# Kernel optimization log

Measured on AMD Instinct MI355X. Metric: run time of the kernel, lower is better.

The kernel has to match this reference:

```python
import jax, jax.numpy as jnp
import numpy as np

H = 16      # hidden_size (fixed by fc1 = Linear(16, 32))
L = 4       # num_layers
F = 256     # feature_size
A = 16      # attention_hidden_size
T = 131072  # seq_len


def setup_inputs() -> dict:
    key = jax.random.key(0)
    ks = jax.random.split(key, 17)
    def g(k, shape, scale=0.1):
        return jax.random.normal(k, shape, dtype=jnp.float32) * scale
    return {
        "batch": jax.random.normal(ks[0], (T, 1, F), dtype=jnp.float32),
        # GRUCell layer 0 (input F -> H), PyTorch layout [3H, in]: r|z|n gates
        "Wih0": g(ks[1], (3 * H, F)), "Whh0": g(ks[2], (3 * H, H)),
        "bih0": g(ks[3], (3 * H,)),   "bhh0": g(ks[4], (3 * H,)),
        # GRUCell layers 1..L-1 (H -> H), stacked
        "Wih": g(ks[5], (L - 1, 3 * H, H)), "Whh": g(ks[6], (L - 1, 3 * H, H)),
        "bih": g(ks[7], (L - 1, 3 * H)),    "bhh": g(ks[8], (L - 1, 3 * H)),
        # additive self-attention combine per layer: v^T tanh(W h + b) + c
        "aW": g(ks[9], (L, H, A)), "ab": g(ks[10], (L, A)),
        "av": g(ks[11], (L, A)),   "avb": g(ks[12], (L,)),
        # head MLP (dropout = identity in eval)
        "fc1W": g(ks[13], (32, H)), "fc1b": g(ks[14], (32,)),
        "fc2W": g(ks[15], (1, 32)), "fc2b": g(ks[16], (1,)),
    }


def _gru(x, h, Wih, Whh, bih, bhh):
    # PyTorch GRUCell math, gates ordered r|z|n
    gi = x @ Wih.T + bih          # [1, 3H]
    gh = h @ Whh.T + bhh          # [1, 3H]
    ir, iz, inn = jnp.split(gi, 3, axis=-1)
    hr, hz, hn = jnp.split(gh, 3, axis=-1)
    r = jax.nn.sigmoid(ir + hr)
    z = jax.nn.sigmoid(iz + hz)
    n = jnp.tanh(inn + r * hn)
    return (1.0 - z) * n + z * h


def reference(batch, Wih0, Whh0, bih0, bhh0, Wih, Whh, bih, bhh,
              aW, ab, av, avb, fc1W, fc1b, fc2W, fc2b):
    def step(hs, x_t):  # hs: [L, 1, H], x_t: [1, F]
        inp = x_t
        new = []
        for l in range(L):  # fixed tiny layer loop, distinct weights
            if l == 0:
                hn = _gru(inp, hs[0], Wih0, Whh0, bih0, bhh0)
            else:
                hn = _gru(inp, hs[l], Wih[l - 1], Whh[l - 1], bih[l - 1], bhh[l - 1])
            new.append(hn)
            inp = hn
        stack = jnp.stack(new)  # [L, 1, H]
        outs = []
        for i in range(L):
            sub = stack[i:]                                        # [L-i, 1, H]
            s = jnp.tanh(sub @ aW[i] + ab[i]) @ av[i] + avb[i]      # [L-i, 1]
            a = jax.nn.softmax(s, axis=0)
            outs.append(jnp.sum(a[..., None] * sub, axis=0))        # [1, H]
        hs_new = jnp.stack(outs)                                    # [L, 1, H]
        top = hs_new[-1][0]                                         # [H]
        o = jax.nn.relu(top @ fc1W.T + fc1b) @ fc2W.T + fc2b        # [1]
        return hs_new, o

    hs0 = jnp.zeros((L, 1, H), dtype=batch.dtype)
    _, ys = jax.lax.scan(step, hs0, batch)
    return ys  # [T, 1]
```

## Files before the change

### kernel.cpp

```cpp
#include <hip/hip_runtime.h>
#include <cstddef>

namespace {
constexpr int kH = 16;
constexpr int kL = 4;
constexpr int kF = 256;
constexpr int kA = 16;
constexpr int kG = 48;
}

#define PIN(x) asm volatile("" : "+v"(x))

#if defined(__has_builtin)
#if __has_builtin(__builtin_amdgcn_permlane16_swap) && __has_builtin(__builtin_amdgcn_permlane32_swap)
#define HAVE_PLSWAP 1
#endif
#endif

#ifdef HAVE_PLSWAP
__device__ __forceinline__ float swap_sum32(float x) {
  auto r = __builtin_amdgcn_permlane32_swap(__float_as_uint(x), __float_as_uint(x), false, false);
  return __uint_as_float(r[0]) + __uint_as_float(r[1]);
}
__device__ __forceinline__ float swap_sum16(float x) {
  auto r = __builtin_amdgcn_permlane16_swap(__float_as_uint(x), __float_as_uint(x), false, false);
  return __uint_as_float(r[0]) + __uint_as_float(r[1]);
}
#else
__device__ __forceinline__ float swap_sum32(float x) {
  return x + __shfl(x, (int)(threadIdx.x & 63) ^ 32, 64);
}
__device__ __forceinline__ float swap_sum16(float x) {
  return x + __shfl(x, (int)(threadIdx.x & 63) ^ 16, 64);
}
#endif

template <int CTRL>
__device__ __forceinline__ float ror_add(float x) {
  int r = __builtin_amdgcn_update_dpp(0, __float_as_int(x), CTRL, 0xF, 0xF, false);
  return x + __int_as_float(r);
}
__device__ __forceinline__ float row_sum16(float x) {
  x = ror_add<0x128>(x);
  x = ror_add<0x124>(x);
  x = ror_add<0x122>(x);
  x = ror_add<0x121>(x);
  return x;
}
__device__ __forceinline__ float fast_rcp(float x) { return __builtin_amdgcn_rcpf(x); }
constexpr float kL2E = 1.4426950408889634f;
__device__ __forceinline__ float sigm(float x) {
  return fast_rcp(1.0f + __builtin_amdgcn_exp2f(-kL2E * x));
}
__device__ __forceinline__ float tanh_f(float x) {
  return 1.0f - 2.0f * fast_rcp(1.0f + __builtin_amdgcn_exp2f((2.0f * kL2E) * x));
}

#define FMAC_ROR(acc, h, w, J)                                            \
  asm volatile("v_fmac_f32_dpp %0, %1, %2 row_ror:" #J                    \
               " row_mask:0xf bank_mask:0xf"                              \
               : "+v"(acc) : "v"(h), "v"(w))
#define MUL_ROR(dst, h, w, J)                                             \
  asm volatile("v_mul_f32_dpp %0, %1, %2 row_ror:" #J                     \
               " row_mask:0xf bank_mask:0xf"                              \
               : "=v"(dst) : "v"(h), "v"(w))

__device__ __forceinline__ float dot16r(const float* w, float h, float bias) {
  float a0, a1, a2, a3;
  asm volatile("v_fma_f32 %0, %1, %2, %3" : "=v"(a0) : "v"(h), "v"(w[0]), "v"(bias));
  asm volatile("s_nop 0" ::: );
  MUL_ROR(a1, h, w[1], 1);
  MUL_ROR(a2, h, w[2], 2);
  MUL_ROR(a3, h, w[3], 3);
  FMAC_ROR(a0, h, w[4], 4);
  FMAC_ROR(a1, h, w[5], 5);
  FMAC_ROR(a2, h, w[6], 6);
  FMAC_ROR(a3, h, w[7], 7);
  FMAC_ROR(a0, h, w[8], 8);
  FMAC_ROR(a1, h, w[9], 9);
  FMAC_ROR(a2, h, w[10], 10);
  FMAC_ROR(a3, h, w[11], 11);
  FMAC_ROR(a0, h, w[12], 12);
  FMAC_ROR(a1, h, w[13], 13);
  FMAC_ROR(a2, h, w[14], 14);
  FMAC_ROR(a3, h, w[15], 15);
  return (a0 + a1) + (a2 + a3);
}

__global__ __launch_bounds__(256) void gi0_kernel(
    const float* __restrict__ batch, const float* __restrict__ Wih0,
    const float* __restrict__ bih0, float* __restrict__ gi0, int T) {
  __shared__ __align__(16) float w[kG * kF];
  __shared__ float bsh[kG];
  for (int i = threadIdx.x; i < kG * kF; i += blockDim.x) w[i] = Wih0[i];
  if (threadIdx.x < kG) bsh[threadIdx.x] = bih0[threadIdx.x];
  __syncthreads();
  int t = blockIdx.x * blockDim.x + threadIdx.x;
  if (t >= T) return;
  float acc[kG];
#pragma unroll
  for (int gg = 0; gg < kG; ++gg) acc[gg] = bsh[gg];
  const float* brow = batch + (size_t)t * kF;
  for (int f = 0; f < kF; f += 4) {
    const float4 b4 = *reinterpret_cast<const float4*>(brow + f);
#pragma unroll
    for (int gg = 0; gg < kG; ++gg) {
      const float4 w4 = *reinterpret_cast<const float4*>(&w[gg * kF + f]);
      acc[gg] = fmaf(b4.x, w4.x, acc[gg]);
      acc[gg] = fmaf(b4.y, w4.y, acc[gg]);
      acc[gg] = fmaf(b4.z, w4.z, acc[gg]);
      acc[gg] = fmaf(b4.w, w4.w, acc[gg]);
    }
  }
  float* orow = gi0 + (size_t)t * kG;
#pragma unroll
  for (int gg = 0; gg < kG; gg += 4) {
    *reinterpret_cast<float4*>(orow + gg) =
        make_float4(acc[gg], acc[gg + 1], acc[gg + 2], acc[gg + 3]);
  }
}

__global__ __launch_bounds__(64)
__attribute__((amdgpu_waves_per_eu(1, 1)))
void seq_kernel(
    const float* __restrict__ Whh0, const float* __restrict__ bhh0,
    const float* __restrict__ Wih, const float* __restrict__ Whh,
    const float* __restrict__ bih, const float* __restrict__ bhh,
    const float* __restrict__ aW, const float* __restrict__ ab,
    const float* __restrict__ av, const float* __restrict__ avb,
    const float* __restrict__ gi0, float* __restrict__ topout, int T) {
  const int lane = threadIdx.x & 63;
  const int grp = lane >> 4;
  const int a = lane & 15;
  const int gr = (grp == 0) ? a : (grp == 2 ? 32 + a : 16 + a);

  float Wh[kL][kH];
  float Ux[3][kH];
  float aWj[kH];
#pragma unroll
  for (int j = 0; j < kH; ++j) {
    const int idx = (a - j) & 15;
    Wh[0][j] = Whh0[gr * kH + idx];
#pragma unroll
    for (int l = 1; l < kL; ++l) {
      Wh[l][j] = Whh[((l - 1) * kG + gr) * kH + idx];
      Ux[l - 1][j] = Wih[((l - 1) * kG + gr) * kH + idx];
    }
    aWj[j] = aW[(grp * kH + idx) * kA + a];
  }
  float bh[kL], bi[3];
  bh[0] = bhh0[gr];
#pragma unroll
  for (int l = 1; l < kL; ++l) {
    bh[l] = bhh[(l - 1) * kG + gr];
    bi[l - 1] = bih[(l - 1) * kG + gr];
  }
  float abr = ab[grp * kA + a];
  float avr = av[grp * kA + a];
  float avbr = avb[grp];

#pragma unroll
  for (int l = 0; l < kL; ++l) {
#pragma unroll
    for (int k = 0; k < kH; ++k) PIN(Wh[l][k]);
    PIN(bh[l]);
  }
#pragma unroll
  for (int l = 0; l < 3; ++l) {
#pragma unroll
    for (int k = 0; k < kH; ++k) PIN(Ux[l][k]);
    PIN(bi[l]);
  }
#pragma unroll
  for (int k = 0; k < kH; ++k) PIN(aWj[k]);
  PIN(abr); PIN(avr); PIN(avbr);

  float hs = 0.0f;
  const float* pG = gi0 + gr;
  float g0 = pG[0], g1 = pG[kG], g2 = pG[2 * kG];

  for (int t = 0; t < T; ++t) {
    const float gcur = g0;
    g0 = g1; g1 = g2;
    {
      int tn = t + 3;
      tn = tn < T ? tn : T - 1;
      g2 = pG[(size_t)tn * kG];
    }

    float hq[kL];
    hq[0] = swap_sum16(swap_sum32(grp == 0 ? hs : 0.0f));
    hq[1] = swap_sum32(swap_sum16(grp == 1 ? hs : 0.0f));
    hq[2] = swap_sum16(swap_sum32(grp == 2 ? hs : 0.0f));
    hq[3] = swap_sum32(swap_sum16(grp == 3 ? hs : 0.0f));

    float xg[kL];
    float sc[kL];

#pragma unroll
    for (int l = 0; l < kL; ++l) {
      const float accH = dot16r(Wh[l], hq[l], bh[l]);
      const float accX = (l == 0) ? gcur : dot16r(Ux[l - 1], xg[l - 1], bi[l - 1]);
      const float sg = sigm(accX + accH);
      const float rv = swap_sum32(grp == 0 ? sg : 0.0f);
      const float zv = swap_sum16(grp == 3 ? sg : 0.0f);
      const float nt = tanh_f(fmaf(rv, accH, accX));
      const float hnew = fmaf(zv, hq[l] - nt, nt);
      xg[l] = swap_sum16(swap_sum32(grp == 2 ? hnew : 0.0f));
      const float d = tanh_f(dot16r(aWj, xg[l], abr));
      sc[l] = row_sum16(d * avr) + avbr;
    }

    const float s0 = (grp == 0) ? sc[0] : -1e30f;
    const float s1 = (grp <= 1) ? sc[1] : -1e30f;
    const float s2 = (grp <= 2) ? sc[2] : -1e30f;
    const float s3 = sc[3];
    const float m = fmaxf(fmaxf(s0, s1), fmaxf(s2, s3));
    const float e0 = __builtin_amdgcn_exp2f((s0 - m) * kL2E);
    const float e1 = __builtin_amdgcn_exp2f((s1 - m) * kL2E);
    const float e2 = __builtin_amdgcn_exp2f((s2 - m) * kL2E);
    const float e3 = __builtin_amdgcn_exp2f((s3 - m) * kL2E);
    const float rden = fast_rcp((e0 + e1) + (e2 + e3));
    float num = e0 * xg[0];
    num = fmaf(e1, xg[1], num);
    num = fmaf(e2, xg[2], num);
    num = fmaf(e3, xg[3], num);
    hs = num * rden;

    if (lane >= 48) topout[(size_t)t * kH + a] = hs;
  }
}

__global__ __launch_bounds__(256) void head_kernel(
    const float* __restrict__ top, const float* __restrict__ fc1W,
    const float* __restrict__ fc1b, const float* __restrict__ fc2W,
    const float* __restrict__ fc2b, float* __restrict__ out, int T) {
  __shared__ __align__(16) float w1[32 * kH];
  __shared__ float b1[32], w2[32];
  for (int i = threadIdx.x; i < 32 * kH; i += blockDim.x) w1[i] = fc1W[i];
  if (threadIdx.x < 32) {
    b1[threadIdx.x] = fc1b[threadIdx.x];
    w2[threadIdx.x] = fc2W[threadIdx.x];
  }
  __syncthreads();
  int t = blockIdx.x * blockDim.x + threadIdx.x;
  if (t >= T) return;
  const float* hrow = top + (size_t)t * kH;
  float hv[kH];
#pragma unroll
  for (int k = 0; k < kH; k += 4) {
    const float4 h4 = *reinterpret_cast<const float4*>(hrow + k);
    hv[k] = h4.x; hv[k + 1] = h4.y; hv[k + 2] = h4.z; hv[k + 3] = h4.w;
  }
  float o = fc2b[0];
#pragma unroll
  for (int mth = 0; mth < 32; ++mth) {
    float acc = b1[mth];
#pragma unroll
    for (int k = 0; k < kH; ++k) acc = fmaf(hv[k], w1[mth * kH + k], acc);
    acc = fmaxf(acc, 0.0f);
    o = fmaf(acc, w2[mth], o);
  }
  out[t] = o;
}

extern "C" void kernel_launch(void* const* d_in, const int* in_sizes, int n_in,
                              void* d_out, int out_size, void* d_ws, size_t ws_size,
                              hipStream_t stream) {
  const float* batch = (const float*)d_in[0];
  const float* Wih0  = (const float*)d_in[1];
  const float* Whh0  = (const float*)d_in[2];
  const float* bih0  = (const float*)d_in[3];
  const float* bhh0  = (const float*)d_in[4];
  const float* Wih   = (const float*)d_in[5];
  const float* Whh   = (const float*)d_in[6];
  const float* bih   = (const float*)d_in[7];
  const float* bhh   = (const float*)d_in[8];
  const float* aW    = (const float*)d_in[9];
  const float* ab    = (const float*)d_in[10];
  const float* av    = (const float*)d_in[11];
  const float* avb   = (const float*)d_in[12];
  const float* fc1W  = (const float*)d_in[13];
  const float* fc1b  = (const float*)d_in[14];
  const float* fc2W  = (const float*)d_in[15];
  const float* fc2b  = (const float*)d_in[16];
  float* out = (float*)d_out;

  const int T = in_sizes[0] / kF;

  float* gi0 = (float*)d_ws;
  float* top = gi0 + (size_t)T * kG;

  const int blocks = (T + 255) / 256;
  gi0_kernel<<<blocks, 256, 0, stream>>>(batch, Wih0, bih0, gi0, T);
  seq_kernel<<<1, 64, 0, stream>>>(Whh0, bhh0, Wih, Whh, bih, bhh,
                                   aW, ab, av, avb, gi0, top, T);
  head_kernel<<<blocks, 256, 0, stream>>>(top, fc1W, fc1b, fc2W, fc2b, out, T);
}
```

Before: 143.8 ms.

## Transpose gi0 and top buffers to time-major and unroll recurrence by four

Stores the precomputed layer-0 input gates and the top hidden states as gate-major/feature-major arrays, so the serial recurrence kernel loads four timesteps of its gate with one float4 and writes four outputs per lane with one float4 store. The sequential loop is unrolled by four steps with prefetching two groups ahead. This cuts per-step global memory instructions on the single-wave critical path. The cost is strided stores in the gi0 producer and strided loads in the head. The loop assumes T is a multiple of four, and any remainder steps would be dropped.

Result: faster. 128.3 ms (-10.8%).

```diff
diff --git a/kernel.cpp b/kernel.cpp
--- a/kernel.cpp
+++ b/kernel.cpp
@@ -89,7 +89,7 @@
 
 __global__ __launch_bounds__(256) void gi0_kernel(
     const float* __restrict__ batch, const float* __restrict__ Wih0,
-    const float* __restrict__ bih0, float* __restrict__ gi0, int T) {
+    const float* __restrict__ bih0, float* __restrict__ gi0T, int T) {
   __shared__ __align__(16) float w[kG * kF];
   __shared__ float bsh[kG];
   for (int i = threadIdx.x; i < kG * kF; i += blockDim.x) w[i] = Wih0[i];
@@ -112,12 +112,8 @@
       acc[gg] = fmaf(b4.w, w4.w, acc[gg]);
     }
   }
-  float* orow = gi0 + (size_t)t * kG;
-#pragma unroll
-  for (int gg = 0; gg < kG; gg += 4) {
-    *reinterpret_cast<float4*>(orow + gg) =
-        make_float4(acc[gg], acc[gg + 1], acc[gg + 2], acc[gg + 3]);
-  }
+#pragma unroll
+  for (int gg = 0; gg < kG; ++gg) gi0T[(size_t)gg * T + t] = acc[gg];
 }
 
 __global__ __launch_bounds__(64)
@@ -128,7 +124,7 @@
     const float* __restrict__ bih, const float* __restrict__ bhh,
     const float* __restrict__ aW, const float* __restrict__ ab,
     const float* __restrict__ av, const float* __restrict__ avb,
-    const float* __restrict__ gi0, float* __restrict__ topout, int T) {
+    const float* __restrict__ gi0T, float* __restrict__ topT, int T) {
   const int lane = threadIdx.x & 63;
   const int grp = lane >> 4;
   const int a = lane & 15;
@@ -176,63 +172,74 @@
   PIN(abr); PIN(avr); PIN(avbr);
 
   float hs = 0.0f;
-  const float* pG = gi0 + gr;
-  float g0 = pG[0], g1 = pG[kG], g2 = pG[2 * kG];
-
-  for (int t = 0; t < T; ++t) {
-    const float gcur = g0;
-    g0 = g1; g1 = g2;
-    {
-      int tn = t + 3;
-      tn = tn < T ? tn : T - 1;
-      g2 = pG[(size_t)tn * kG];
+
+  const float* pG = gi0T + (size_t)gr * T;
+  float* pT = topT + (size_t)a * T;
+
+  const int NG = T / 4;
+  float4 c4 = *reinterpret_cast<const float4*>(pG + 0);
+  float4 n4 = *reinterpret_cast<const float4*>(pG + 4);
+
+#define STEP(gcur, tslot)                                                     \
+  {                                                                           \
+    float hq[kL];                                                             \
+    hq[0] = swap_sum16(swap_sum32(grp == 0 ? hs : 0.0f));                     \
+    hq[1] = swap_sum32(swap_sum16(grp == 1 ? hs : 0.0f));                     \
+    hq[2] = swap_sum16(swap_sum32(grp == 2 ? hs : 0.0f));                     \
+    hq[3] = swap_sum32(swap_sum16(grp == 3 ? hs : 0.0f));                     \
+    float xg[kL];                                                             \
+    float sc[kL];                                                             \
+    _Pragma("unroll")                                                         \
+    for (int l = 0; l < kL; ++l) {                                            \
+      const float accH = dot16r(Wh[l], hq[l], bh[l]);                         \
+      const float accX = (l == 0) ? (gcur)                                    \
+                                  : dot16r(Ux[l - 1], xg[l - 1], bi[l - 1]);  \
+      const float sg = sigm(accX + accH);                                     \
+      const float rv = swap_sum32(grp == 0 ? sg : 0.0f);                      \
+      const float zv = swap_sum16(grp == 3 ? sg : 0.0f);                      \
+      const float nt = tanh_f(fmaf(rv, accH, accX));                          \
+      const float hnew = fmaf(zv, hq[l] - nt, nt);                            \
+      xg[l] = swap_sum16(swap_sum32(grp == 2 ? hnew : 0.0f));                 \
+      const float d = tanh_f(dot16r(aWj, xg[l], abr));                        \
+      sc[l] = row_sum16(d * avr) + avbr;                                      \
+    }                                                                         \
+    const float s0 = (grp == 0) ? sc[0] : -1e30f;                             \
+    const float s1 = (grp <= 1) ? sc[1] : -1e30f;                             \
+    const float s2 = (grp <= 2) ? sc[2] : -1e30f;                             \
+    const float s3 = sc[3];                                                   \
+    const float m = fmaxf(fmaxf(s0, s1), fmaxf(s2, s3));                      \
+    const float e0 = __builtin_amdgcn_exp2f((s0 - m) * kL2E);                 \
+    const float e1 = __builtin_amdgcn_exp2f((s1 - m) * kL2E);                 \
+    const float e2 = __builtin_amdgcn_exp2f((s2 - m) * kL2E);                 \
+    const float e3 = __builtin_amdgcn_exp2f((s3 - m) * kL2E);                 \
+    const float rden = fast_rcp((e0 + e1) + (e2 + e3));                       \
+    float num = e0 * xg[0];                                                   \
+    num = fmaf(e1, xg[1], num);                                               \
+    num = fmaf(e2, xg[2], num);                                               \
+    num = fmaf(e3, xg[3], num);                                               \
+    hs = num * rden;                                                          \
+    tslot = hs;                                                               \
+  }
+
+  for (int g = 0; g < NG; ++g) {
+    const int gn = (g + 2 < NG) ? g + 2 : NG - 1;
+    const float4 t4 = *reinterpret_cast<const float4*>(pG + (size_t)gn * 4);
+    float o0, o1, o2, o3;
+    STEP(c4.x, o0)
+    STEP(c4.y, o1)
+    STEP(c4.z, o2)
+    STEP(c4.w, o3)
+    if (lane >= 48) {
+      *reinterpret_cast<float4*>(pT + (size_t)g * 4) = make_float4(o0, o1, o2, o3);
     }
-
-    float hq[kL];
-    hq[0] = swap_sum16(swap_sum32(grp == 0 ? hs : 0.0f));
-    hq[1] = swap_sum32(swap_sum16(grp == 1 ? hs : 0.0f));
-    hq[2] = swap_sum16(swap_sum32(grp == 2 ? hs : 0.0f));
-    hq[3] = swap_sum32(swap_sum16(grp == 3 ? hs : 0.0f));
-
-    float xg[kL];
-    float sc[kL];
-
-#pragma unroll
-    for (int l = 0; l < kL; ++l) {
-      const float accH = dot16r(Wh[l], hq[l], bh[l]);
-      const float accX = (l == 0) ? gcur : dot16r(Ux[l - 1], xg[l - 1], bi[l - 1]);
-      const float sg = sigm(accX + accH);
-      const float rv = swap_sum32(grp == 0 ? sg : 0.0f);
-      const float zv = swap_sum16(grp == 3 ? sg : 0.0f);
-      const float nt = tanh_f(fmaf(rv, accH, accX));
-      const float hnew = fmaf(zv, hq[l] - nt, nt);
-      xg[l] = swap_sum16(swap_sum32(grp == 2 ? hnew : 0.0f));
-      const float d = tanh_f(dot16r(aWj, xg[l], abr));
-      sc[l] = row_sum16(d * avr) + avbr;
-    }
-
-    const float s0 = (grp == 0) ? sc[0] : -1e30f;
-    const float s1 = (grp <= 1) ? sc[1] : -1e30f;
-    const float s2 = (grp <= 2) ? sc[2] : -1e30f;
-    const float s3 = sc[3];
-    const float m = fmaxf(fmaxf(s0, s1), fmaxf(s2, s3));
-    const float e0 = __builtin_amdgcn_exp2f((s0 - m) * kL2E);
-    const float e1 = __builtin_amdgcn_exp2f((s1 - m) * kL2E);
-    const float e2 = __builtin_amdgcn_exp2f((s2 - m) * kL2E);
-    const float e3 = __builtin_amdgcn_exp2f((s3 - m) * kL2E);
-    const float rden = fast_rcp((e0 + e1) + (e2 + e3));
-    float num = e0 * xg[0];
-    num = fmaf(e1, xg[1], num);
-    num = fmaf(e2, xg[2], num);
-    num = fmaf(e3, xg[3], num);
-    hs = num * rden;
-
-    if (lane >= 48) topout[(size_t)t * kH + a] = hs;
-  }
+    c4 = n4;
+    n4 = t4;
+  }
+#undef STEP
 }
 
 __global__ __launch_bounds__(256) void head_kernel(
-    const float* __restrict__ top, const float* __restrict__ fc1W,
+    const float* __restrict__ topT, const float* __restrict__ fc1W,
     const float* __restrict__ fc1b, const float* __restrict__ fc2W,
     const float* __restrict__ fc2b, float* __restrict__ out, int T) {
   __shared__ __align__(16) float w1[32 * kH];
@@ -245,13 +252,9 @@
   __syncthreads();
   int t = blockIdx.x * blockDim.x + threadIdx.x;
   if (t >= T) return;
-  const float* hrow = top + (size_t)t * kH;
   float hv[kH];
 #pragma unroll
-  for (int k = 0; k < kH; k += 4) {
-    const float4 h4 = *reinterpret_cast<const float4*>(hrow + k);
-    hv[k] = h4.x; hv[k + 1] = h4.y; hv[k + 2] = h4.z; hv[k + 3] = h4.w;
-  }
+  for (int k = 0; k < kH; ++k) hv[k] = topT[(size_t)k * T + t];
   float o = fc2b[0];
 #pragma unroll
   for (int mth = 0; mth < 32; ++mth) {
@@ -288,12 +291,12 @@
 
   const int T = in_sizes[0] / kF;
 
-  float* gi0 = (float*)d_ws;
-  float* top = gi0 + (size_t)T * kG;
+  float* gi0T = (float*)d_ws;
+  float* topT = gi0T + (size_t)kG * T;
 
   const int blocks = (T + 255) / 256;
-  gi0_kernel<<<blocks, 256, 0, stream>>>(batch, Wih0, bih0, gi0, T);
+  gi0_kernel<<<blocks, 256, 0, stream>>>(batch, Wih0, bih0, gi0T, T);
   seq_kernel<<<1, 64, 0, stream>>>(Whh0, bhh0, Wih, Whh, bih, bhh,
-                                   aW, ab, av, avb, gi0, top, T);
-  head_kernel<<<blocks, 256, 0, stream>>>(top, fc1W, fc1b, fc2W, fc2b, out, T);
-}
+                                   aW, ab, av, avb, gi0T, topT, T);
+  head_kernel<<<blocks, 256, 0, stream>>>(topT, fc1W, fc1b, fc2W, fc2b, out, T);
+}
```
